# Optimization experiments

Measured on AMD Instinct MI355X. Metric: run time of the kernel, lower is better.

Reference implementation:

```python
import jax, jax.numpy as jnp
import numpy as np

NEG = -100000000.0  # NOT_POSSIBLE_TRANSITION
B, T, F, NT = 64, 512, 1024, 50
H = NT + 2  # +2 for start/stop tags
START, STOP = H - 2, H - 1


def setup_inputs() -> dict:
    key = jax.random.key(0)
    k0, k1, k2, k3 = jax.random.split(key, 4)
    features = jax.random.normal(k0, (B, T, F), jnp.float32)
    tags = jax.random.randint(k1, (B, T), 0, NT)
    masks = jnp.ones((B, T), jnp.float32)
    W = jax.random.normal(k2, (H, F), jnp.float32) * 0.02  # nn.Linear weight
    b = jnp.zeros((H,), jnp.float32)                        # nn.Linear bias
    transition = jax.random.normal(k3, (H, H), jnp.float32)
    transition = transition.at[START, :].set(NEG).at[:, STOP].set(NEG)
    return dict(features=features, W=W, b=b, transition=transition,
                masks=masks, tags=tags)


def _forward_algorithm(emit, masks, transition):
    # emit: [B,T,H], masks: [B,T]
    b_, _, h = emit.shape
    init = jnp.full((b_, h), NEG, emit.dtype).at[:, START].set(0.0)

    def step(scores, xs):
        emit_t, mask_t = xs  # [B,H], [B]
        # score_t[b, i] = logsumexp_j(scores[b,j] + transition[i,j] + emit_t[b,i])
        s = scores[:, None, :] + transition[None, :, :] + emit_t[:, :, None]
        s = jax.nn.logsumexp(s, axis=-1)
        m = mask_t[:, None]
        scores = s * m + scores * (1.0 - m)
        return scores, None

    scores, _ = jax.lax.scan(step, init, (emit.transpose(1, 0, 2), masks.T))
    return jax.nn.logsumexp(scores + transition[STOP], axis=-1)  # [B]


def _gold_score(emit, tags, masks, transition):
    b_ = emit.shape[0]
    emit_sc = jnp.take_along_axis(emit, tags[:, :, None], axis=2)[:, :, 0]  # [B,T]
    start = jnp.full((b_, 1), START, tags.dtype)
    tags_ext = jnp.concatenate([start, tags], axis=1)  # [B,T+1]
    trans_sc = transition[tags_ext[:, 1:], tags_ext[:, :-1]]  # [B,T]
    last_pos = masks.sum(axis=1).astype(jnp.int32)  # index into tags_ext
    last_tag = jnp.take_along_axis(tags_ext, last_pos[:, None], axis=1)[:, 0]
    last_score = transition[STOP, last_tag]
    return ((trans_sc + emit_sc) * masks).sum(axis=1) + last_score  # [B]


def reference(features, W, b, transition, masks, tags):
    emit = features @ W.T + b  # [B,T,H]
    fwd = _forward_algorithm(emit, masks, transition)
    gold = _gold_score(emit, tags, masks, transition)
    return (fwd - gold).mean()  # CRF NLL loss (scalar)


if __name__ == "__main__":
    print(reference(**setup_inputs()))
```

## Files before the change

kernel.cpp:

```cpp
#include <hip/hip_runtime.h>
#include <hip/hip_bf16.h>
#include <math.h>


#define NEGV   (-100000000.0f)
#define BB     64
#define TT     512
#define FF     1024
#define HH     52
#define HP     64
#define S_START 50
#define S_STOP  51
#define NCH    32
#define CLEN   (TT / NCH)
#define GRP    8
#define NGRP   (NCH / GRP)

typedef __bf16 bf16x8 __attribute__((ext_vector_type(8)));
typedef __bf16 bf16x4 __attribute__((ext_vector_type(4)));
typedef float  f32x4  __attribute__((ext_vector_type(4)));

#define WS_CHUNK  0u
#define WS_CEXP   16777216u
#define WS_GBUF   16785408u
#define WS_GCEXP  18882560u
#define WS_WBF    18883584u
#define WS_EXPT   19014656u
#define WS_GOLD   19022848u

__global__ __launch_bounds__(256) void k_prep(const float* __restrict__ W,
                                              const float* __restrict__ trans,
                                              __bf16* __restrict__ wbf,
                                              __bf16* __restrict__ expT,
                                              float* __restrict__ gold) {
  int n = blockIdx.x;
  if (n == 0) {
    if (threadIdx.x < BB) gold[threadIdx.x] = 0.0f;
    for (int idx = threadIdx.x; idx < 4096; idx += 256) {
      int m = idx >> 6, k = idx & 63;
      float tv = (k >= HH) ? NEGV : ((m >= HH) ? 0.0f : trans[m * HH + k]);
      expT[idx] = (__bf16)__expf(tv);
    }
  }
  for (int k = threadIdx.x; k < FF; k += 256) {
    float v = (n < HH) ? W[n * FF + k] : 0.0f;
    wbf[n * FF + k] = (__bf16)v;
  }
}

__global__ __launch_bounds__(256, 2) void k_scan(const float* __restrict__ feat,
                                                 const __bf16* __restrict__ wbf,
                                                 const __bf16* __restrict__ expT,
                                                 const float* __restrict__ bias,
                                                 const float* __restrict__ trans,
                                                 const float* __restrict__ masks,
                                                 const int* __restrict__ tags,
                                                 __bf16* __restrict__ chunks,
                                                 float* __restrict__ cexp,
                                                 float* __restrict__ gold) {
  const int tid = threadIdx.x;
  const int wv = tid >> 6;
  const int l  = tid & 63;
  const int lm = l & 15;
  const int q  = l >> 4;
  const int chunk = blockIdx.x * 4 + wv;
  const int b = chunk >> 5, c = chunk & 31;

  __shared__ __align__(16) __bf16 PTall[4][64 * 72];
  __shared__ __align__(16) __bf16 Eall[4][CLEN * 64];
  __bf16* pt = PTall[wv];
  __bf16* el = Eall[wv];

  const float* fbase = feat + ((size_t)(b * TT + c * CLEN)) * FF;
  const float* arow  = fbase + (size_t)lm * FF + q * 8;

  f32x4 apre[4][2];
#pragma unroll
  for (int s = 0; s < 4; ++s)
#pragma unroll
    for (int h = 0; h < 2; ++h)
      apre[s][h] = *(const f32x4*)(arow + s * 32 + h * 4);

  bf16x8 bcur[4];
#pragma unroll
  for (int nt = 0; nt < 4; ++nt)
    bcur[nt] = *(const bf16x8*)(wbf + (size_t)(nt * 16 + lm) * FF + q * 8);

  f32x4 acc[4] = {};

#pragma unroll
  for (int kt = 0; kt < 32; ++kt) {
    const int st = kt & 3;
    bf16x8 af;
#pragma unroll
    for (int j = 0; j < 4; ++j) {
      af[j]     = (__bf16)apre[st][0][j];
      af[4 + j] = (__bf16)apre[st][1][j];
    }
    if (kt + 4 < 32) {
#pragma unroll
      for (int h = 0; h < 2; ++h)
        apre[st][h] = *(const f32x4*)(arow + (kt + 4) * 32 + h * 4);
    }
    bf16x8 bnx[4];
    if (kt + 1 < 32) {
#pragma unroll
      for (int nt = 0; nt < 4; ++nt)
        bnx[nt] = *(const bf16x8*)(wbf + (size_t)(nt * 16 + lm) * FF + (kt + 1) * 32 + q * 8);
    }
#pragma unroll
    for (int nt = 0; nt < 4; ++nt)
      acc[nt] = __builtin_amdgcn_mfma_f32_16x16x32_bf16(af, bcur[nt], acc[nt], 0, 0, 0);
    if (kt + 1 < 32) {
#pragma unroll
      for (int nt = 0; nt < 4; ++nt) bcur[nt] = bnx[nt];
    }
  }

#pragma unroll
  for (int nt = 0; nt < 4; ++nt) {
    int n = nt * 16 + lm;
    float bn = (n < HH) ? bias[n] : 0.0f;
#pragma unroll
    for (int rr = 0; rr < 4; ++rr)
      el[(q * 4 + rr) * 64 + n] = (__bf16)(acc[nt][rr] + bn);
  }

  float mreg = (l < CLEN) ? masks[b * TT + c * CLEN + l] : 1.0f;
  int cur = (l < CLEN) ? tags[b * TT + c * CLEN + l] : 0;
  int prev = __shfl_up(cur, 1);
  if (l == 0) prev = (c == 0) ? S_START : tags[b * TT + c * CLEN - 1];
  float gp = 0.0f;
  if (l < CLEN) {
    float e  = (float)el[l * 64 + cur];
    float tr = trans[cur * HH + prev];
    gp = (e + tr) * mreg;
  }
#pragma unroll
  for (int d = 1; d < 64; d <<= 1) gp += __shfl_xor(gp, d);
  if (l == 0) atomicAdd(&gold[b], gp);

  bf16x8 afrag[4][2];
#pragma unroll
  for (int mt = 0; mt < 4; ++mt)
#pragma unroll
    for (int kk = 0; kk < 2; ++kk)
      afrag[mt][kk] = *(const bf16x8*)&expT[(mt * 16 + lm) * 64 + kk * 32 + q * 8];

  for (int idx = l; idx < 4096; idx += 64) {
    int n = idx >> 6, mm = idx & 63;
    pt[n * 72 + mm] = (__bf16)((n == mm) ? 1.0f : 0.0f);
  }

  int eacc = 0, rpend = 0;
  const float LOG2E = 1.4426950408889634f;

  for (int t = 0; t < CLEN; ++t) {
    float mcur = __shfl(mreg, t);
    if (mcur != 0.0f) {
      float sh = (float)(7 + rpend);
      eacc += 7 + rpend;
      rpend = 0;
      float s[4][4];
#pragma unroll
      for (int mt = 0; mt < 4; ++mt) {
        bf16x4 em4 = *(const bf16x4*)&el[t * 64 + mt * 16 + q * 4];
#pragma unroll
        for (int rr = 0; rr < 4; ++rr)
          s[mt][rr] = __builtin_amdgcn_exp2f(fmaf((float)em4[rr], LOG2E, -sh));
      }

      bf16x8 bfr[2][4];
#pragma unroll
      for (int kk = 0; kk < 2; ++kk)
#pragma unroll
        for (int nt = 0; nt < 4; ++nt)
          bfr[kk][nt] = *(const bf16x8*)&pt[(nt * 16 + lm) * 72 + kk * 32 + q * 8];

      const bool trk = ((t & 7) == 7) && (t != CLEN - 1);
      float lmax = 0.0f;
      f32x4 zero = {};
#pragma unroll
      for (int mt = 0; mt < 4; ++mt) {
#pragma unroll
        for (int nt = 0; nt < 4; ++nt) {
          f32x4 a = __builtin_amdgcn_mfma_f32_16x16x32_bf16(afrag[mt][0], bfr[0][nt], zero, 0, 0, 0);
          a = __builtin_amdgcn_mfma_f32_16x16x32_bf16(afrag[mt][1], bfr[1][nt], a, 0, 0, 0);
          bf16x4 w4;
#pragma unroll
          for (int rr = 0; rr < 4; ++rr) {
            float v = a[rr] * s[mt][rr];
            if (trk) lmax = fmaxf(lmax, v);
            w4[rr] = (__bf16)v;
          }
          *(bf16x4*)&pt[(nt * 16 + lm) * 72 + mt * 16 + q * 4] = w4;
        }
      }
      if (trk) {
#pragma unroll
        for (int d = 1; d < 64; d <<= 1) lmax = fmaxf(lmax, __shfl_xor(lmax, d));
        if (lmax > 0.0f) rpend = ilogbf(lmax);
      }
    }
  }

  __bf16* cb = chunks + (size_t)chunk * 4096;
#pragma unroll
  for (int it = 0; it < 8; ++it) {
    bf16x8 v;
#pragma unroll
    for (int e = 0; e < 8; ++e) v[e] = pt[(it * 8 + e) * 72 + l];
    *(bf16x8*)&cb[it * 512 + l * 8] = v;
  }
  if (l == 0) cexp[chunk] = (float)eacc;
}

__global__ __launch_bounds__(64) void k_ga(const __bf16* __restrict__ chunks,
                                           const float* __restrict__ cexp,
                                           __bf16* __restrict__ gbuf,
                                           float* __restrict__ gcexp) {
  const int g  = blockIdx.x;
  const int b  = g >> 2, qq = g & 3;
  const int l  = threadIdx.x;
  const int lm = l & 15;
  const int q  = l >> 4;

  __shared__ __align__(16) __bf16 ptq[64 * 72];
  const __bf16* mbase = chunks + ((size_t)(b * NCH + qq * GRP)) * 4096;

#pragma unroll
  for (int it = 0; it < 8; ++it) {
    bf16x8 mv = *(const bf16x8*)&mbase[it * 512 + l * 8];
#pragma unroll
    for (int e = 0; e < 8; ++e) ptq[(it * 8 + e) * 72 + l] = mv[e];
  }

#pragma unroll
  for (int j = 1; j < GRP; ++j) {
    const __bf16* mj = mbase + (size_t)j * 4096;
    bf16x8 af[4][2];
#pragma unroll
    for (int mt = 0; mt < 4; ++mt)
#pragma unroll
      for (int kk = 0; kk < 2; ++kk)
        af[mt][kk] = *(const bf16x8*)&mj[(kk * 4 + q) * 512 + (mt * 16 + lm) * 8];
    bf16x8 bfr[2][4];
#pragma unroll
    for (int kk = 0; kk < 2; ++kk)
#pragma unroll
      for (int nt = 0; nt < 4; ++nt)
        bfr[kk][nt] = *(const bf16x8*)&ptq[(nt * 16 + lm) * 72 + kk * 32 + q * 8];
    f32x4 zero = {};
#pragma unroll
    for (int mt = 0; mt < 4; ++mt) {
#pragma unroll
      for (int nt = 0; nt < 4; ++nt) {
        f32x4 a = __builtin_amdgcn_mfma_f32_16x16x32_bf16(af[mt][0], bfr[0][nt], zero, 0, 0, 0);
        a = __builtin_amdgcn_mfma_f32_16x16x32_bf16(af[mt][1], bfr[1][nt], a, 0, 0, 0);
        bf16x4 w4;
#pragma unroll
        for (int rr = 0; rr < 4; ++rr) w4[rr] = (__bf16)a[rr];
        *(bf16x4*)&ptq[(nt * 16 + lm) * 72 + mt * 16 + q * 4] = w4;
      }
    }
  }

  float vals[8][8];
  float lmax = 0.0f;
#pragma unroll
  for (int it = 0; it < 8; ++it)
#pragma unroll
    for (int e = 0; e < 8; ++e) {
      float x = (float)ptq[(it * 8 + e) * 72 + l];
      vals[it][e] = x;
      lmax = fmaxf(lmax, x);
    }
#pragma unroll
  for (int d = 1; d < 64; d <<= 1) lmax = fmaxf(lmax, __shfl_xor(lmax, d));
  int ee = (lmax > 0.0f) ? ilogbf(lmax) : 0;
  float sc = ldexpf(1.0f, -ee);
  __bf16* gb = gbuf + (size_t)g * 4096;
#pragma unroll
  for (int it = 0; it < 8; ++it) {
    bf16x8 w;
#pragma unroll
    for (int e = 0; e < 8; ++e) w[e] = (__bf16)(vals[it][e] * sc);
    *(bf16x8*)&gb[it * 512 + l * 8] = w;
  }
  if (l == 0) {
    float s = (float)ee;
#pragma unroll
    for (int c = 0; c < GRP; ++c) s += cexp[b * NCH + qq * GRP + c];
    gcexp[g] = s;
  }
}

__global__ __launch_bounds__(64) void k_gb(const __bf16* __restrict__ gbuf,
                                           const float* __restrict__ gcexp,
                                           const float* __restrict__ trans,
                                           const float* __restrict__ masks,
                                           const int* __restrict__ tags,
                                           const float* __restrict__ gold,
                                           float* __restrict__ out) {
  const int b = blockIdx.x;
  const int l = threadIdx.x;
  __shared__ __align__(16) float vsh[64];
  float v = (l == S_START) ? 1.0f : 0.0f;
  float esum = 0.0f;
  const float LN2 = 0.6931471805599453f;

  float msum = 0.0f;
  for (int t = l; t < TT; t += 64) msum += masks[b * TT + t];

  bf16x8 pf[NGRP][8];
#pragma unroll
  for (int p = 0; p < NGRP; ++p)
#pragma unroll
    for (int it = 0; it < 8; ++it)
      pf[p][it] = *(const bf16x8*)&gbuf[((size_t)(b * NGRP + p)) * 4096 + it * 512 + l * 8];

#pragma unroll
  for (int g = 0; g < NGRP; ++g) {
    vsh[l] = v;
    float u = 0.0f;
#pragma unroll
    for (int it = 0; it < 8; ++it) {
      bf16x8 m8 = pf[g][it];
      f32x4 va = *(const f32x4*)&vsh[it * 8];
      f32x4 vb = *(const f32x4*)&vsh[it * 8 + 4];
      u += (float)m8[0] * va[0] + (float)m8[1] * va[1]
         + (float)m8[2] * va[2] + (float)m8[3] * va[3]
         + (float)m8[4] * vb[0] + (float)m8[5] * vb[1]
         + (float)m8[6] * vb[2] + (float)m8[7] * vb[3];
    }
    esum += gcexp[b * NGRP + g] * LN2;
    float mxx = u;
#pragma unroll
    for (int d = 1; d < 64; d <<= 1) mxx = fmaxf(mxx, __shfl_xor(mxx, d));
    if (mxx > 0.0f) {
      int ee = ilogbf(mxx);
      u = ldexpf(u, -ee);
      esum += (float)ee * LN2;
    }
    v = u;
  }

  float ts = (l < HH) ? trans[S_STOP * HH + l] : NEGV;
  float contrib = v * __expf(ts);
#pragma unroll
  for (int d = 1; d < 64; d <<= 1) {
    contrib += __shfl_xor(contrib, d);
    msum += __shfl_xor(msum, d);
  }
  if (l == 0) {
    int lp = (int)(msum + 0.5f);
    int lt = (lp == 0) ? S_START : tags[b * TT + lp - 1];
    float goldb = gold[b] + trans[S_STOP * HH + lt];
    float fwd = __logf(contrib) + esum;
    atomicAdd(out, (fwd - goldb) * (1.0f / 64.0f));
  }
}

extern "C" void kernel_launch(void* const* d_in, const int* in_sizes, int n_in,
                              void* d_out, int out_size, void* d_ws, size_t ws_size,
                              hipStream_t stream) {
  (void)in_sizes; (void)n_in; (void)out_size; (void)ws_size;
  const float* feat  = (const float*)d_in[0];
  const float* W     = (const float*)d_in[1];
  const float* bias  = (const float*)d_in[2];
  const float* trans = (const float*)d_in[3];
  const float* masks = (const float*)d_in[4];
  const int*   tags  = (const int*)d_in[5];

  char* ws = (char*)d_ws;
  __bf16* chunks = (__bf16*)(ws + WS_CHUNK);
  float*  cexp   = (float*)(ws + WS_CEXP);
  __bf16* gbuf   = (__bf16*)(ws + WS_GBUF);
  float*  gcexp  = (float*)(ws + WS_GCEXP);
  __bf16* wbf    = (__bf16*)(ws + WS_WBF);
  __bf16* expT   = (__bf16*)(ws + WS_EXPT);
  float*  gold   = (float*)(ws + WS_GOLD);

  hipMemsetAsync(d_out, 0, sizeof(float), stream);
  k_prep<<<HP, 256, 0, stream>>>(W, trans, wbf, expT, gold);
  k_scan<<<(BB * NCH) / 4, 256, 0, stream>>>(feat, wbf, expT, bias, trans, masks,
                                             tags, chunks, cexp, gold);
  k_ga<<<BB * NGRP, 64, 0, stream>>>(chunks, cexp, gbuf, gcexp);
  k_gb<<<BB, 64, 0, stream>>>(gbuf, gcexp, trans, masks, tags, gold, (float*)d_out);
}
```

Baseline: 257.7 us.

## Split each scan chunk across four waves with split-K GEMM and column-split scan

Each block now processes a single chunk with four waves instead of four independent chunks. The emission GEMM is split along K across the waves and the partial sums are reduced through shared memory. The serial per-timestep transfer-matrix product is split by column tile so each wave issues a quarter of the MFMAs. The goal is to shorten the latency-bound per-chunk serial chain and launch more blocks. In exchange it adds block barriers and shared-memory traffic, and the rescale-max check now runs only once per chunk (at step 7) and is shared across waves.

```diff
diff --git a/kernel.cpp b/kernel.cpp
--- a/kernel.cpp
+++ b/kernel.cpp
@@ -48,7 +48,7 @@
   }
 }
 
-__global__ __launch_bounds__(256, 2) void k_scan(const float* __restrict__ feat,
+__global__ __launch_bounds__(256, 4) void k_scan(const float* __restrict__ feat,
                                                  const __bf16* __restrict__ wbf,
                                                  const __bf16* __restrict__ expT,
                                                  const float* __restrict__ bias,
@@ -63,16 +63,17 @@
   const int l  = tid & 63;
   const int lm = l & 15;
   const int q  = l >> 4;
-  const int chunk = blockIdx.x * 4 + wv;
+  const int chunk = blockIdx.x;
   const int b = chunk >> 5, c = chunk & 31;
 
-  __shared__ __align__(16) __bf16 PTall[4][64 * 72];
-  __shared__ __align__(16) __bf16 Eall[4][CLEN * 64];
-  __bf16* pt = PTall[wv];
-  __bf16* el = Eall[wv];
+  __shared__ __align__(16) float  POOL[4 * 1024];
+  __shared__ __align__(16) __bf16 el[CLEN * 64];
+  __shared__ float maxsh[4];
+  float*  pstage = POOL;
+  __bf16* pt     = (__bf16*)POOL;
 
   const float* fbase = feat + ((size_t)(b * TT + c * CLEN)) * FF;
-  const float* arow  = fbase + (size_t)lm * FF + q * 8;
+  const float* arow  = fbase + (size_t)lm * FF + wv * 256 + q * 8;
 
   f32x4 apre[4][2];
 #pragma unroll
@@ -84,12 +85,12 @@
   bf16x8 bcur[4];
 #pragma unroll
   for (int nt = 0; nt < 4; ++nt)
-    bcur[nt] = *(const bf16x8*)(wbf + (size_t)(nt * 16 + lm) * FF + q * 8);
+    bcur[nt] = *(const bf16x8*)(wbf + (size_t)(nt * 16 + lm) * FF + wv * 256 + q * 8);
 
   f32x4 acc[4] = {};
 
 #pragma unroll
-  for (int kt = 0; kt < 32; ++kt) {
+  for (int kt = 0; kt < 8; ++kt) {
     const int st = kt & 3;
     bf16x8 af;
 #pragma unroll
@@ -97,48 +98,66 @@
       af[j]     = (__bf16)apre[st][0][j];
       af[4 + j] = (__bf16)apre[st][1][j];
     }
-    if (kt + 4 < 32) {
+    if (kt + 4 < 8) {
 #pragma unroll
       for (int h = 0; h < 2; ++h)
         apre[st][h] = *(const f32x4*)(arow + (kt + 4) * 32 + h * 4);
     }
     bf16x8 bnx[4];
-    if (kt + 1 < 32) {
+    if (kt + 1 < 8) {
 #pragma unroll
       for (int nt = 0; nt < 4; ++nt)
-        bnx[nt] = *(const bf16x8*)(wbf + (size_t)(nt * 16 + lm) * FF + (kt + 1) * 32 + q * 8);
+        bnx[nt] = *(const bf16x8*)(wbf + (size_t)(nt * 16 + lm) * FF + wv * 256 + (kt + 1) * 32 + q * 8);
     }
 #pragma unroll
     for (int nt = 0; nt < 4; ++nt)
       acc[nt] = __builtin_amdgcn_mfma_f32_16x16x32_bf16(af, bcur[nt], acc[nt], 0, 0, 0);
-    if (kt + 1 < 32) {
+    if (kt + 1 < 8) {
 #pragma unroll
       for (int nt = 0; nt < 4; ++nt) bcur[nt] = bnx[nt];
     }
   }
 
 #pragma unroll
-  for (int nt = 0; nt < 4; ++nt) {
-    int n = nt * 16 + lm;
-    float bn = (n < HH) ? bias[n] : 0.0f;
+  for (int nt = 0; nt < 4; ++nt)
 #pragma unroll
     for (int rr = 0; rr < 4; ++rr)
-      el[(q * 4 + rr) * 64 + n] = (__bf16)(acc[nt][rr] + bn);
-  }
+      pstage[wv * 1024 + (q * 4 + rr) * 64 + nt * 16 + lm] = acc[nt][rr];
+  __syncthreads();
+
+  {
+    const int base = tid * 4;
+    const int n0 = (tid & 15) * 4;
+    f32x4 s0 = *(const f32x4*)&pstage[base];
+    f32x4 s1 = *(const f32x4*)&pstage[1024 + base];
+    f32x4 s2 = *(const f32x4*)&pstage[2048 + base];
+    f32x4 s3 = *(const f32x4*)&pstage[3072 + base];
+    bf16x4 w;
+#pragma unroll
+    for (int j = 0; j < 4; ++j) {
+      int n = n0 + j;
+      float bn = (n < HH) ? bias[n] : 0.0f;
+      w[j] = (__bf16)(s0[j] + s1[j] + s2[j] + s3[j] + bn);
+    }
+    *(bf16x4*)&el[base] = w;
+  }
+  __syncthreads();
 
   float mreg = (l < CLEN) ? masks[b * TT + c * CLEN + l] : 1.0f;
-  int cur = (l < CLEN) ? tags[b * TT + c * CLEN + l] : 0;
-  int prev = __shfl_up(cur, 1);
-  if (l == 0) prev = (c == 0) ? S_START : tags[b * TT + c * CLEN - 1];
-  float gp = 0.0f;
-  if (l < CLEN) {
-    float e  = (float)el[l * 64 + cur];
-    float tr = trans[cur * HH + prev];
-    gp = (e + tr) * mreg;
-  }
-#pragma unroll
-  for (int d = 1; d < 64; d <<= 1) gp += __shfl_xor(gp, d);
-  if (l == 0) atomicAdd(&gold[b], gp);
+  if (wv == 0) {
+    int cur = (l < CLEN) ? tags[b * TT + c * CLEN + l] : 0;
+    int prev = __shfl_up(cur, 1);
+    if (l == 0) prev = (c == 0) ? S_START : tags[b * TT + c * CLEN - 1];
+    float gp = 0.0f;
+    if (l < CLEN) {
+      float e  = (float)el[l * 64 + cur];
+      float tr = trans[cur * HH + prev];
+      gp = (e + tr) * mreg;
+    }
+#pragma unroll
+    for (int d = 1; d < 64; d <<= 1) gp += __shfl_xor(gp, d);
+    if (l == 0) atomicAdd(&gold[b], gp);
+  }
 
   bf16x8 afrag[4][2];
 #pragma unroll
@@ -147,9 +166,10 @@
     for (int kk = 0; kk < 2; ++kk)
       afrag[mt][kk] = *(const bf16x8*)&expT[(mt * 16 + lm) * 64 + kk * 32 + q * 8];
 
-  for (int idx = l; idx < 4096; idx += 64) {
-    int n = idx >> 6, mm = idx & 63;
-    pt[n * 72 + mm] = (__bf16)((n == mm) ? 1.0f : 0.0f);
+#pragma unroll
+  for (int r = 0; r < 16; ++r) {
+    int j = wv * 16 + r;
+    pt[j * 72 + l] = (__bf16)((j == l) ? 1.0f : 0.0f);
   }
 
   int eacc = 0, rpend = 0;
@@ -170,49 +190,48 @@
           s[mt][rr] = __builtin_amdgcn_exp2f(fmaf((float)em4[rr], LOG2E, -sh));
       }
 
-      bf16x8 bfr[2][4];
+      bf16x8 bfr[2];
 #pragma unroll
       for (int kk = 0; kk < 2; ++kk)
-#pragma unroll
-        for (int nt = 0; nt < 4; ++nt)
-          bfr[kk][nt] = *(const bf16x8*)&pt[(nt * 16 + lm) * 72 + kk * 32 + q * 8];
-
-      const bool trk = ((t & 7) == 7) && (t != CLEN - 1);
+        bfr[kk] = *(const bf16x8*)&pt[(wv * 16 + lm) * 72 + kk * 32 + q * 8];
+
+      const bool trk = (t == 7);
       float lmax = 0.0f;
       f32x4 zero = {};
 #pragma unroll
       for (int mt = 0; mt < 4; ++mt) {
-#pragma unroll
-        for (int nt = 0; nt < 4; ++nt) {
-          f32x4 a = __builtin_amdgcn_mfma_f32_16x16x32_bf16(afrag[mt][0], bfr[0][nt], zero, 0, 0, 0);
-          a = __builtin_amdgcn_mfma_f32_16x16x32_bf16(afrag[mt][1], bfr[1][nt], a, 0, 0, 0);
-          bf16x4 w4;
-#pragma unroll
-          for (int rr = 0; rr < 4; ++rr) {
-            float v = a[rr] * s[mt][rr];
-            if (trk) lmax = fmaxf(lmax, v);
-            w4[rr] = (__bf16)v;
-          }
-          *(bf16x4*)&pt[(nt * 16 + lm) * 72 + mt * 16 + q * 4] = w4;
+        f32x4 a = __builtin_amdgcn_mfma_f32_16x16x32_bf16(afrag[mt][0], bfr[0], zero, 0, 0, 0);
+        a = __builtin_amdgcn_mfma_f32_16x16x32_bf16(afrag[mt][1], bfr[1], a, 0, 0, 0);
+        bf16x4 w4;
+#pragma unroll
+        for (int rr = 0; rr < 4; ++rr) {
+          float v = a[rr] * s[mt][rr];
+          if (trk) lmax = fmaxf(lmax, v);
+          w4[rr] = (__bf16)v;
         }
+        *(bf16x4*)&pt[(wv * 16 + lm) * 72 + mt * 16 + q * 4] = w4;
       }
       if (trk) {
 #pragma unroll
         for (int d = 1; d < 64; d <<= 1) lmax = fmaxf(lmax, __shfl_xor(lmax, d));
-        if (lmax > 0.0f) rpend = ilogbf(lmax);
+        if (l == 0) maxsh[wv] = lmax;
+        __syncthreads();
+        float m4 = fmaxf(fmaxf(maxsh[0], maxsh[1]), fmaxf(maxsh[2], maxsh[3]));
+        if (m4 > 0.0f) rpend = ilogbf(m4);
       }
     }
   }
 
   __bf16* cb = chunks + (size_t)chunk * 4096;
 #pragma unroll
-  for (int it = 0; it < 8; ++it) {
+  for (int i2 = 0; i2 < 2; ++i2) {
+    int it = wv * 2 + i2;
     bf16x8 v;
 #pragma unroll
     for (int e = 0; e < 8; ++e) v[e] = pt[(it * 8 + e) * 72 + l];
     *(bf16x8*)&cb[it * 512 + l * 8] = v;
   }
-  if (l == 0) cexp[chunk] = (float)eacc;
+  if (tid == 0) cexp[chunk] = (float)eacc;
 }
 
 __global__ __launch_bounds__(64) void k_ga(const __bf16* __restrict__ chunks,
@@ -383,8 +402,8 @@
 
   hipMemsetAsync(d_out, 0, sizeof(float), stream);
   k_prep<<<HP, 256, 0, stream>>>(W, trans, wbf, expT, gold);
-  k_scan<<<(BB * NCH) / 4, 256, 0, stream>>>(feat, wbf, expT, bias, trans, masks,
-                                             tags, chunks, cexp, gold);
+  k_scan<<<BB * NCH, 256, 0, stream>>>(feat, wbf, expT, bias, trans, masks,
+                                       tags, chunks, cexp, gold);
   k_ga<<<BB * NGRP, 64, 0, stream>>>(chunks, cexp, gbuf, gcexp);
   k_gb<<<BB, 64, 0, stream>>>(gbuf, gcexp, trans, masks, tags, gold, (float*)d_out);
 }
```

After: 258.6 us. Within noise of the previous version (+0.4%).
